# Kernel optimization log

Hardware: AMD Instinct MI355X
Metric: run time of the kernel (lower is better)

Reference implementation:

```python
import jax, jax.numpy as jnp
import numpy as np

HEADSIZE = 64  # Attention 'channels' arg: per-head dim used by split_heads and the scale


def setup_inputs() -> dict:
    key = jax.random.key(0)
    # [B, C, T, H, W]; C must equal channels*heads = 512 (channel_split constraint)
    x = jax.random.normal(key, (4, 512, 8, 14, 14), dtype=jnp.float32)
    return {"x": x}


def _attention(x):
    # qkv = SplitIdentity(3): repeat along channels then split back -> q = k = v = x
    B, C, T, H, W = x.shape
    N = T * H * W
    # Tokenizer.tokenize with token_dim=None: permute(0, T, H, W, C) -> [B, N, C]
    tok = jnp.transpose(x, (0, 2, 3, 4, 1)).reshape(B, N, C)
    # split_heads: reshape(B, N, headsize, heads).permute(0, 3, 1, 2) -> [B, h, N, d]
    q = tok.reshape(B, N, HEADSIZE, -1).transpose(0, 3, 1, 2)
    # qkv_aggregate: double scaling (q*s) @ (k^T * s), softmax, @ v ; s = d**-0.5
    scale = HEADSIZE ** -0.5
    scores = jnp.einsum('bhnd,bhmd->bhnm', q * scale, q * scale)  # [B,h,N,N]
    attn = jax.nn.softmax(scores, axis=-1)
    out = jnp.einsum('bhnm,bhmd->bhnd', attn, q)
    # merge_heads: permute(0, 2, 3, 1).reshape(B, N, d*h) — inverse of split_heads
    merged = out.transpose(0, 2, 3, 1).reshape(B, N, C)
    # untokenize: [B, T, H, W, C] -> [B, C, T, H, W]; proj = identity, dropouts p=0
    return merged.reshape(B, T, H, W, C).transpose(0, 4, 1, 2, 3)


def reference(x):
    return _attention(x)
```

## Files before the change

kernel.cpp:

```cpp
#include <hip/hip_runtime.h>

typedef _Float16 f16x8 __attribute__((ext_vector_type(8)));
typedef _Float16 f16x4 __attribute__((ext_vector_type(4)));
typedef __fp16   fp16x2 __attribute__((ext_vector_type(2)));
typedef float    f32x4 __attribute__((ext_vector_type(4)));
typedef unsigned int u32x4 __attribute__((ext_vector_type(4)));

constexpr int NTOK   = 1568;
constexpr int NHEADS = 8;
constexpr int NCH    = 512;
constexpr int NC32   = 52;
constexpr float SK   = 0.15014030f;
constexpr size_t IMG_BH = (size_t)NC32 * 4096;

__global__ __launch_bounds__(256)
void prep_kernel(const float* __restrict__ x, char* __restrict__ Kimg, char* __restrict__ Vimg)
{
    const int bh = blockIdx.x, c32 = blockIdx.y;
    const int b = bh >> 3, h = bh & 7;
    const int t = threadIdx.x;
    const int f = t >> 6, l = t & 63, l15 = l & 15, grp = l >> 4;

    char* Kg = Kimg + (size_t)bh * IMG_BH + (size_t)(c32 * 4 + f) * 1024 + l * 16;
    char* Vg = Vimg + (size_t)bh * IMG_BH + (size_t)(c32 * 4 + f) * 1024 + l * 16;

    const int n0 = c32 * 32;
    if (n0 >= NTOK) {
        f16x8 z;
#pragma unroll
        for (int j = 0; j < 8; ++j) z[j] = (_Float16)0.f;
        *(f16x8*)Kg = z; *(f16x8*)Vg = z;
        return;
    }

    __shared__ _Float16 kbuf[32][72];
    __shared__ _Float16 vbuf[64][40];

    const int tok = t & 31, dhi = t >> 5;
#pragma unroll
    for (int p = 0; p < 8; ++p) {
        const int d = 8 * p + dhi;
        const float v = x[((size_t)b * NCH + d * NHEADS + h) * NTOK + n0 + tok];
        kbuf[tok][d] = (_Float16)(v * SK);
        vbuf[d][tok] = (_Float16)v;
    }
    __syncthreads();

    *(f16x8*)Kg = *(const f16x8*)&kbuf[(f >> 1) * 16 + l15][(f & 1) * 32 + grp * 8];
    f16x4 va = *(const f16x4*)&vbuf[f * 16 + l15][4 * grp];
    f16x4 vb = *(const f16x4*)&vbuf[f * 16 + l15][16 + 4 * grp];
    f16x8 vv;
#pragma unroll
    for (int j = 0; j < 4; ++j) { vv[j] = va[j]; vv[4 + j] = vb[j]; }
    *(f16x8*)Vg = vv;
}

static __device__ __forceinline__ f16x8 make_bp(f32x4 sA, f32x4 sB)
{
    u32x4 w;
    w[0] = __builtin_bit_cast(unsigned int,
        __builtin_amdgcn_cvt_pkrtz(__builtin_amdgcn_exp2f(sA[0]), __builtin_amdgcn_exp2f(sA[1])));
    w[1] = __builtin_bit_cast(unsigned int,
        __builtin_amdgcn_cvt_pkrtz(__builtin_amdgcn_exp2f(sA[2]), __builtin_amdgcn_exp2f(sA[3])));
    w[2] = __builtin_bit_cast(unsigned int,
        __builtin_amdgcn_cvt_pkrtz(__builtin_amdgcn_exp2f(sB[0]), __builtin_amdgcn_exp2f(sB[1])));
    w[3] = __builtin_bit_cast(unsigned int,
        __builtin_amdgcn_cvt_pkrtz(__builtin_amdgcn_exp2f(sB[2]), __builtin_amdgcn_exp2f(sB[3])));
    return __builtin_bit_cast(f16x8, w);
}

__global__ __launch_bounds__(256, 3)
void attn_fwd(const char* __restrict__ Kimg, const char* __restrict__ Vimg,
              float* __restrict__ out)
{
    const int orig = blockIdx.x;
    const int wgid = (orig & 7) * 100 + (orig >> 3);
    const int qt = wgid % 25, bh = wgid / 25;
    const int b = bh >> 3, head = bh & 7;
    const int t = threadIdx.x, kw = t >> 6, lane = t & 63;
    const int l15 = lane & 15, grp = lane >> 4;

    const char* Kb = Kimg + (size_t)bh * IMG_BH;
    const char* Vb = Vimg + (size_t)bh * IMG_BH;

    f16x8 aq[4][2];
#pragma unroll
    for (int sub = 0; sub < 4; ++sub)
#pragma unroll
        for (int ks = 0; ks < 2; ++ks)
            aq[sub][ks] = *(const f16x8*)(Kb + (size_t)((qt * 4 + sub) * 2 + ks) * 1024 + lane * 16);

    f16x8 ones;
#pragma unroll
    for (int j = 0; j < 8; ++j) ones[j] = (_Float16)1.f;

    f32x4 oacc[4][4];
    f32x4 lacc[4];
#pragma unroll
    for (int s = 0; s < 4; ++s) {
        lacc[s] = f32x4{0.f, 0.f, 0.f, 0.f};
#pragma unroll
        for (int db = 0; db < 4; ++db) oacc[s][db] = f32x4{0.f, 0.f, 0.f, 0.f};
    }

    const int start = (kw == 0) ? 0 : 13 + (kw - 1) * 12;
    const int nc    = (kw == 0) ? 13 : 12;
    const f32x4 z4 = {0.f, 0.f, 0.f, 0.f};

    for (int i = 0; i < nc; ++i) {
        const int c32 = start + i;
        const char* kbase = Kb + (size_t)c32 * 4096 + lane * 16;
        const char* vbase = Vb + (size_t)c32 * 4096 + lane * 16;

        f16x8 ka0 = *(const f16x8*)(kbase);
        f16x8 ka1 = *(const f16x8*)(kbase + 1024);
        f16x8 kb0 = *(const f16x8*)(kbase + 2048);
        f16x8 kb1 = *(const f16x8*)(kbase + 3072);
        f16x8 vf0 = *(const f16x8*)(vbase);
        f16x8 vf1 = *(const f16x8*)(vbase + 1024);
        f16x8 vf2 = *(const f16x8*)(vbase + 2048);
        f16x8 vf3 = *(const f16x8*)(vbase + 3072);

#pragma unroll
        for (int sub = 0; sub < 4; ++sub) {
            f32x4 sA = __builtin_amdgcn_mfma_f32_16x16x32_f16(ka0, aq[sub][0], z4, 0, 0, 0);
            sA = __builtin_amdgcn_mfma_f32_16x16x32_f16(ka1, aq[sub][1], sA, 0, 0, 0);
            f32x4 sB = __builtin_amdgcn_mfma_f32_16x16x32_f16(kb0, aq[sub][0], z4, 0, 0, 0);
            sB = __builtin_amdgcn_mfma_f32_16x16x32_f16(kb1, aq[sub][1], sB, 0, 0, 0);
            const f16x8 bp = make_bp(sA, sB);
            lacc[sub]    = __builtin_amdgcn_mfma_f32_16x16x32_f16(ones, bp, lacc[sub], 0, 0, 0);
            oacc[sub][0] = __builtin_amdgcn_mfma_f32_16x16x32_f16(vf0, bp, oacc[sub][0], 0, 0, 0);
            oacc[sub][1] = __builtin_amdgcn_mfma_f32_16x16x32_f16(vf1, bp, oacc[sub][1], 0, 0, 0);
            oacc[sub][2] = __builtin_amdgcn_mfma_f32_16x16x32_f16(vf2, bp, oacc[sub][2], 0, 0, 0);
            oacc[sub][3] = __builtin_amdgcn_mfma_f32_16x16x32_f16(vf3, bp, oacc[sub][3], 0, 0, 0);
        }
    }

    __shared__ float comb[64][69];
    for (int r = 1; r < 4; ++r) {
        if (kw == r) {
#pragma unroll
            for (int s = 0; s < 4; ++s) {
#pragma unroll
                for (int db = 0; db < 4; ++db)
#pragma unroll
                    for (int q = 0; q < 4; ++q) comb[lane][s * 16 + db * 4 + q] = oacc[s][db][q];
                comb[lane][64 + s] = lacc[s][0];
            }
        }
        __syncthreads();
        if (kw == 0) {
#pragma unroll
            for (int s = 0; s < 4; ++s) {
#pragma unroll
                for (int db = 0; db < 4; ++db)
#pragma unroll
                    for (int q = 0; q < 4; ++q) oacc[s][db][q] += comb[lane][s * 16 + db * 4 + q];
                lacc[s][0] += comb[lane][64 + s];
            }
        }
        __syncthreads();
    }

    if (kw == 0) {
#pragma unroll
        for (int sub = 0; sub < 4; ++sub) {
            const int qrow = qt * 64 + sub * 16 + l15;
            if (qrow < NTOK) {
                const float inv = 1.0f / lacc[sub][0];
#pragma unroll
                for (int db = 0; db < 4; ++db)
#pragma unroll
                    for (int q = 0; q < 4; ++q) {
                        const int d = db * 16 + 4 * grp + q;
                        out[((size_t)b * NCH + (size_t)d * NHEADS + head) * NTOK + qrow] = oacc[sub][db][q] * inv;
                    }
            }
        }
    }
}

extern "C" void kernel_launch(void* const* d_in, const int* in_sizes, int n_in,
                              void* d_out, int out_size, void* d_ws, size_t ws_size,
                              hipStream_t stream)
{
    const float* x = (const float*)d_in[0];
    float* out     = (float*)d_out;

    char* Kimg = (char*)d_ws;
    char* Vimg = (char*)d_ws + 32 * IMG_BH;

    dim3 pgrid(32, NC32);
    prep_kernel<<<pgrid, 256, 0, stream>>>(x, Kimg, Vimg);

    attn_fwd<<<800, 256, 0, stream>>>(Kimg, Vimg, out);
}
```

Baseline: 43.20 us.

## Switch attention to 32x32x16 MFMA with 32-row query tiles

Replaces the 16x16x32 MFMA tiling with 32x32x16 MFMA instructions. The K/V images are relaid out in the prep kernel to match the new operand layout. Each block now handles 32 query rows instead of 64, so the grid grows from 800 to 1568 blocks and register use for accumulators drops. This is meant to use the larger MFMA shape more efficiently and raise occupancy. In exchange, each block reuses K/V across fewer queries, so global K/V traffic doubles.

After: 46.40 us. 1.07x slower.

```diff
diff --git a/kernel.cpp b/kernel.cpp
--- a/kernel.cpp
+++ b/kernel.cpp
@@ -2,8 +2,8 @@
 
 typedef _Float16 f16x8 __attribute__((ext_vector_type(8)));
 typedef _Float16 f16x4 __attribute__((ext_vector_type(4)));
-typedef __fp16   fp16x2 __attribute__((ext_vector_type(2)));
 typedef float    f32x4 __attribute__((ext_vector_type(4)));
+typedef float    f32x16 __attribute__((ext_vector_type(16)));
 typedef unsigned int u32x4 __attribute__((ext_vector_type(4)));
 
 constexpr int NTOK   = 1568;
@@ -19,7 +19,7 @@
     const int bh = blockIdx.x, c32 = blockIdx.y;
     const int b = bh >> 3, h = bh & 7;
     const int t = threadIdx.x;
-    const int f = t >> 6, l = t & 63, l15 = l & 15, grp = l >> 4;
+    const int f = t >> 6, l = t & 63, l31 = l & 31, g = l >> 5;
 
     char* Kg = Kimg + (size_t)bh * IMG_BH + (size_t)(c32 * 4 + f) * 1024 + l * 16;
     char* Vg = Vimg + (size_t)bh * IMG_BH + (size_t)(c32 * 4 + f) * 1024 + l * 16;
@@ -46,27 +46,16 @@
     }
     __syncthreads();
 
-    *(f16x8*)Kg = *(const f16x8*)&kbuf[(f >> 1) * 16 + l15][(f & 1) * 32 + grp * 8];
-    f16x4 va = *(const f16x4*)&vbuf[f * 16 + l15][4 * grp];
-    f16x4 vb = *(const f16x4*)&vbuf[f * 16 + l15][16 + 4 * grp];
+    *(f16x8*)Kg = *(const f16x8*)&kbuf[l31][16 * f + 8 * g];
+
+    const int dv = 32 * (f >> 1) + l31;
+    const int tb = 4 * g + 16 * (f & 1);
+    f16x4 va = *(const f16x4*)&vbuf[dv][tb];
+    f16x4 vb = *(const f16x4*)&vbuf[dv][tb + 8];
     f16x8 vv;
 #pragma unroll
     for (int j = 0; j < 4; ++j) { vv[j] = va[j]; vv[4 + j] = vb[j]; }
     *(f16x8*)Vg = vv;
-}
-
-static __device__ __forceinline__ f16x8 make_bp(f32x4 sA, f32x4 sB)
-{
-    u32x4 w;
-    w[0] = __builtin_bit_cast(unsigned int,
-        __builtin_amdgcn_cvt_pkrtz(__builtin_amdgcn_exp2f(sA[0]), __builtin_amdgcn_exp2f(sA[1])));
-    w[1] = __builtin_bit_cast(unsigned int,
-        __builtin_amdgcn_cvt_pkrtz(__builtin_amdgcn_exp2f(sA[2]), __builtin_amdgcn_exp2f(sA[3])));
-    w[2] = __builtin_bit_cast(unsigned int,
-        __builtin_amdgcn_cvt_pkrtz(__builtin_amdgcn_exp2f(sB[0]), __builtin_amdgcn_exp2f(sB[1])));
-    w[3] = __builtin_bit_cast(unsigned int,
-        __builtin_amdgcn_cvt_pkrtz(__builtin_amdgcn_exp2f(sB[2]), __builtin_amdgcn_exp2f(sB[3])));
-    return __builtin_bit_cast(f16x8, w);
 }
 
 __global__ __launch_bounds__(256, 3)
@@ -74,108 +63,105 @@
               float* __restrict__ out)
 {
     const int orig = blockIdx.x;
-    const int wgid = (orig & 7) * 100 + (orig >> 3);
-    const int qt = wgid % 25, bh = wgid / 25;
+    const int wgid = (orig & 7) * 196 + (orig >> 3);
+    const int qt = wgid % 49, bh = wgid / 49;
     const int b = bh >> 3, head = bh & 7;
     const int t = threadIdx.x, kw = t >> 6, lane = t & 63;
-    const int l15 = lane & 15, grp = lane >> 4;
+    const int l31 = lane & 31, g = lane >> 5;
 
     const char* Kb = Kimg + (size_t)bh * IMG_BH;
     const char* Vb = Vimg + (size_t)bh * IMG_BH;
 
-    f16x8 aq[4][2];
-#pragma unroll
-    for (int sub = 0; sub < 4; ++sub)
-#pragma unroll
-        for (int ks = 0; ks < 2; ++ks)
-            aq[sub][ks] = *(const f16x8*)(Kb + (size_t)((qt * 4 + sub) * 2 + ks) * 1024 + lane * 16);
+    f16x8 aq0 = *(const f16x8*)(Kb + (size_t)(qt * 4 + 0) * 1024 + lane * 16);
+    f16x8 aq1 = *(const f16x8*)(Kb + (size_t)(qt * 4 + 1) * 1024 + lane * 16);
+    f16x8 aq2 = *(const f16x8*)(Kb + (size_t)(qt * 4 + 2) * 1024 + lane * 16);
+    f16x8 aq3 = *(const f16x8*)(Kb + (size_t)(qt * 4 + 3) * 1024 + lane * 16);
 
     f16x8 ones;
 #pragma unroll
     for (int j = 0; j < 8; ++j) ones[j] = (_Float16)1.f;
 
-    f32x4 oacc[4][4];
-    f32x4 lacc[4];
+    f32x16 oacc0, oacc1, lacc;
 #pragma unroll
-    for (int s = 0; s < 4; ++s) {
-        lacc[s] = f32x4{0.f, 0.f, 0.f, 0.f};
-#pragma unroll
-        for (int db = 0; db < 4; ++db) oacc[s][db] = f32x4{0.f, 0.f, 0.f, 0.f};
-    }
+    for (int r = 0; r < 16; ++r) { oacc0[r] = 0.f; oacc1[r] = 0.f; lacc[r] = 0.f; }
 
     const int start = (kw == 0) ? 0 : 13 + (kw - 1) * 12;
     const int nc    = (kw == 0) ? 13 : 12;
-    const f32x4 z4 = {0.f, 0.f, 0.f, 0.f};
+    f32x16 z16;
+#pragma unroll
+    for (int r = 0; r < 16; ++r) z16[r] = 0.f;
 
     for (int i = 0; i < nc; ++i) {
         const int c32 = start + i;
         const char* kbase = Kb + (size_t)c32 * 4096 + lane * 16;
         const char* vbase = Vb + (size_t)c32 * 4096 + lane * 16;
 
-        f16x8 ka0 = *(const f16x8*)(kbase);
-        f16x8 ka1 = *(const f16x8*)(kbase + 1024);
-        f16x8 kb0 = *(const f16x8*)(kbase + 2048);
-        f16x8 kb1 = *(const f16x8*)(kbase + 3072);
-        f16x8 vf0 = *(const f16x8*)(vbase);
-        f16x8 vf1 = *(const f16x8*)(vbase + 1024);
-        f16x8 vf2 = *(const f16x8*)(vbase + 2048);
-        f16x8 vf3 = *(const f16x8*)(vbase + 3072);
+        f16x8 kf0 = *(const f16x8*)(kbase);
+        f16x8 kf1 = *(const f16x8*)(kbase + 1024);
+        f16x8 kf2 = *(const f16x8*)(kbase + 2048);
+        f16x8 kf3 = *(const f16x8*)(kbase + 3072);
+        f16x8 vf00 = *(const f16x8*)(vbase);
+        f16x8 vf01 = *(const f16x8*)(vbase + 1024);
+        f16x8 vf10 = *(const f16x8*)(vbase + 2048);
+        f16x8 vf11 = *(const f16x8*)(vbase + 3072);
 
-#pragma unroll
-        for (int sub = 0; sub < 4; ++sub) {
-            f32x4 sA = __builtin_amdgcn_mfma_f32_16x16x32_f16(ka0, aq[sub][0], z4, 0, 0, 0);
-            sA = __builtin_amdgcn_mfma_f32_16x16x32_f16(ka1, aq[sub][1], sA, 0, 0, 0);
-            f32x4 sB = __builtin_amdgcn_mfma_f32_16x16x32_f16(kb0, aq[sub][0], z4, 0, 0, 0);
-            sB = __builtin_amdgcn_mfma_f32_16x16x32_f16(kb1, aq[sub][1], sB, 0, 0, 0);
-            const f16x8 bp = make_bp(sA, sB);
-            lacc[sub]    = __builtin_amdgcn_mfma_f32_16x16x32_f16(ones, bp, lacc[sub], 0, 0, 0);
-            oacc[sub][0] = __builtin_amdgcn_mfma_f32_16x16x32_f16(vf0, bp, oacc[sub][0], 0, 0, 0);
-            oacc[sub][1] = __builtin_amdgcn_mfma_f32_16x16x32_f16(vf1, bp, oacc[sub][1], 0, 0, 0);
-            oacc[sub][2] = __builtin_amdgcn_mfma_f32_16x16x32_f16(vf2, bp, oacc[sub][2], 0, 0, 0);
-            oacc[sub][3] = __builtin_amdgcn_mfma_f32_16x16x32_f16(vf3, bp, oacc[sub][3], 0, 0, 0);
-        }
+        f32x16 sacc = __builtin_amdgcn_mfma_f32_32x32x16_f16(kf0, aq0, z16, 0, 0, 0);
+        sacc = __builtin_amdgcn_mfma_f32_32x32x16_f16(kf1, aq1, sacc, 0, 0, 0);
+        sacc = __builtin_amdgcn_mfma_f32_32x32x16_f16(kf2, aq2, sacc, 0, 0, 0);
+        sacc = __builtin_amdgcn_mfma_f32_32x32x16_f16(kf3, aq3, sacc, 0, 0, 0);
+
+        u32x4 w0, w1;
+        w0[0] = __builtin_bit_cast(unsigned int, __builtin_amdgcn_cvt_pkrtz(
+                    __builtin_amdgcn_exp2f(sacc[0]), __builtin_amdgcn_exp2f(sacc[1])));
+        w0[1] = __builtin_bit_cast(unsigned int, __builtin_amdgcn_cvt_pkrtz(
+                    __builtin_amdgcn_exp2f(sacc[2]), __builtin_amdgcn_exp2f(sacc[3])));
+        w0[2] = __builtin_bit_cast(unsigned int, __builtin_amdgcn_cvt_pkrtz(
+                    __builtin_amdgcn_exp2f(sacc[4]), __builtin_amdgcn_exp2f(sacc[5])));
+        w0[3] = __builtin_bit_cast(unsigned int, __builtin_amdgcn_cvt_pkrtz(
+                    __builtin_amdgcn_exp2f(sacc[6]), __builtin_amdgcn_exp2f(sacc[7])));
+        w1[0] = __builtin_bit_cast(unsigned int, __builtin_amdgcn_cvt_pkrtz(
+                    __builtin_amdgcn_exp2f(sacc[8]), __builtin_amdgcn_exp2f(sacc[9])));
+        w1[1] = __builtin_bit_cast(unsigned int, __builtin_amdgcn_cvt_pkrtz(
+                    __builtin_amdgcn_exp2f(sacc[10]), __builtin_amdgcn_exp2f(sacc[11])));
+        w1[2] = __builtin_bit_cast(unsigned int, __builtin_amdgcn_cvt_pkrtz(
+                    __builtin_amdgcn_exp2f(sacc[12]), __builtin_amdgcn_exp2f(sacc[13])));
+        w1[3] = __builtin_bit_cast(unsigned int, __builtin_amdgcn_cvt_pkrtz(
+                    __builtin_amdgcn_exp2f(sacc[14]), __builtin_amdgcn_exp2f(sacc[15])));
+        const f16x8 bp0 = __builtin_bit_cast(f16x8, w0);
+        const f16x8 bp1 = __builtin_bit_cast(f16x8, w1);
+
+        lacc  = __builtin_amdgcn_mfma_f32_32x32x16_f16(ones, bp0, lacc, 0, 0, 0);
+        lacc  = __builtin_amdgcn_mfma_f32_32x32x16_f16(ones, bp1, lacc, 0, 0, 0);
+        oacc0 = __builtin_amdgcn_mfma_f32_32x32x16_f16(vf00, bp0, oacc0, 0, 0, 0);
+        oacc0 = __builtin_amdgcn_mfma_f32_32x32x16_f16(vf01, bp1, oacc0, 0, 0, 0);
+        oacc1 = __builtin_amdgcn_mfma_f32_32x32x16_f16(vf10, bp0, oacc1, 0, 0, 0);
+        oacc1 = __builtin_amdgcn_mfma_f32_32x32x16_f16(vf11, bp1, oacc1, 0, 0, 0);
     }
 
-    __shared__ float comb[64][69];
+    __shared__ float comb[64][33];
     for (int r = 1; r < 4; ++r) {
         if (kw == r) {
 #pragma unroll
-            for (int s = 0; s < 4; ++s) {
-#pragma unroll
-                for (int db = 0; db < 4; ++db)
-#pragma unroll
-                    for (int q = 0; q < 4; ++q) comb[lane][s * 16 + db * 4 + q] = oacc[s][db][q];
-                comb[lane][64 + s] = lacc[s][0];
-            }
+            for (int j = 0; j < 16; ++j) { comb[lane][j] = oacc0[j]; comb[lane][16 + j] = oacc1[j]; }
+            comb[lane][32] = lacc[0];
         }
         __syncthreads();
         if (kw == 0) {
 #pragma unroll
-            for (int s = 0; s < 4; ++s) {
-#pragma unroll
-                for (int db = 0; db < 4; ++db)
-#pragma unroll
-                    for (int q = 0; q < 4; ++q) oacc[s][db][q] += comb[lane][s * 16 + db * 4 + q];
-                lacc[s][0] += comb[lane][64 + s];
-            }
+            for (int j = 0; j < 16; ++j) { oacc0[j] += comb[lane][j]; oacc1[j] += comb[lane][16 + j]; }
+            lacc[0] += comb[lane][32];
         }
         __syncthreads();
     }
 
     if (kw == 0) {
+        const int qrow = qt * 32 + l31;
+        const float inv = 1.0f / lacc[0];
 #pragma unroll
-        for (int sub = 0; sub < 4; ++sub) {
-            const int qrow = qt * 64 + sub * 16 + l15;
-            if (qrow < NTOK) {
-                const float inv = 1.0f / lacc[sub][0];
-#pragma unroll
-                for (int db = 0; db < 4; ++db)
-#pragma unroll
-                    for (int q = 0; q < 4; ++q) {
-                        const int d = db * 16 + 4 * grp + q;
-                        out[((size_t)b * NCH + (size_t)d * NHEADS + head) * NTOK + qrow] = oacc[sub][db][q] * inv;
-                    }
-            }
+        for (int r = 0; r < 16; ++r) {
+            const int drow = (r & 3) + 8 * (r >> 2) + 4 * g;
+            out[((size_t)b * NCH + (size_t)(drow * NHEADS) + head) * NTOK + qrow] = oacc0[r] * inv;
+            out[((size_t)b * NCH + (size_t)((32 + drow) * NHEADS) + head) * NTOK + qrow] = oacc1[r] * inv;
         }
     }
 }
@@ -193,5 +179,5 @@
     dim3 pgrid(32, NC32);
     prep_kernel<<<pgrid, 256, 0, stream>>>(x, Kimg, Vimg);
 
-    attn_fwd<<<800, 256, 0, stream>>>(Kimg, Vimg, out);
+    attn_fwd<<<1568, 256, 0, stream>>>(Kimg, Vimg, out);
 }
```
